# Performance work log

Hardware: AMD Instinct MI355X
Metric: run time of the kernel (lower is better)

Reference implementation:

```python
import jax, jax.numpy as jnp
from jax import lax
import numpy as np

T_STEPS, C_IN, H_IN, W_IN = 15, 6, 256, 256
C_OUT, KSIZE = 64, 5
THRESH = 15.0   # conv_t[0]
KWTA = 5        # ks[0]
INH_R = 3       # inh_radiuses[0]


def setup_inputs() -> dict:
    key = jax.random.key(0)
    k1, k2 = jax.random.split(key)
    # cumulative binary spike-wave: once a unit spikes it stays on (SpykeTorch convention)
    bern = jax.random.uniform(k1, (T_STEPS, C_IN, H_IN, W_IN)) < 0.05
    spikes = (jnp.cumsum(bern.astype(jnp.int32), axis=0) > 0).astype(jnp.float32)
    # SpykeTorch Convolution init: N(0.8, 0.05)
    w1 = 0.8 + 0.05 * jax.random.normal(k2, (C_OUT, C_IN, KSIZE, KSIZE), dtype=jnp.float32)
    return {"input": spikes, "w1": w1, "current_layer_id": 1}


def pointwise_inhibition(thr_pot):
    # thr_pot: (T, C, H, W). Keep, at each spatial position, only the feature
    # with the earliest spike (ties broken by max potential); zero the rest.
    T = thr_pot.shape[0]
    C = thr_pot.shape[1]
    max_vals = jnp.max(thr_pot, axis=1, keepdims=True)            # (T,1,H,W)
    max_idx = jnp.argmax(thr_pot, axis=1, keepdims=True)          # (T,1,H,W)
    clamp_pot = jnp.sign(max_vals)                                # (T,1,H,W) in {0,1}
    earliest = jnp.clip((T - clamp_pot.sum(axis=0, keepdims=True)).astype(jnp.int32), 0, T - 1)  # (1,1,H,W)
    winners = jnp.take_along_axis(max_idx, earliest, axis=0)      # (1,1,H,W)
    onehot = (jnp.arange(C)[None, :, None, None] == winners[:, 0])  # (1,C,H,W)
    coef = onehot.astype(thr_pot.dtype) * clamp_pot[-1:]          # zero where no spike at last step
    return thr_pot * coef


def get_k_winners(pot, spk, kwta, inh_radius):
    # pot, spk: (T, C, H, W). Returns (kwta, 3) int winners (c, h, w); -1 rows = no winner.
    T, C, H, W = pot.shape
    earliest = jnp.clip((T - spk.sum(axis=0, keepdims=True)).astype(jnp.int32), 0, T - 1)
    values = jnp.take_along_axis(pot, earliest, axis=0)           # (1,C,H,W)
    trunc = spk * values
    v = trunc.max() * T
    trunc = trunc + spk * v
    total = trunc.sum(axis=0)                                     # (C,H,W)
    rows = jnp.arange(H)
    cols = jnp.arange(W)

    def step(total, _):
        idx = jnp.argmax(total)
        val = total.reshape(-1)[idx]
        c = idx // (H * W)
        rem = idx % (H * W)
        h = rem // W
        w = rem % W
        winner = jnp.where(val != 0,
                           jnp.stack([c, h, w]),
                           jnp.full((3,), -1, dtype=idx.dtype))
        total = total.at[c].set(0.0)
        box = (((rows >= h - inh_radius) & (rows <= h + inh_radius))[:, None]
               & ((cols >= w - inh_radius) & (cols <= w + inh_radius))[None, :])
        total = jnp.where(box[None, :, :], 0.0, total)            # columnar spatial inhibition
        return total, winner

    _, winners = lax.scan(step, total, None, length=kwta)
    return winners


def reference(input, w1, current_layer_id):
    # training path, current_layer_id == 1
    x = jnp.pad(input.astype(jnp.float32), ((0, 0), (0, 0), (2, 2), (2, 2)))  # sf.pad (2,2,2,2)
    pot = lax.conv_general_dilated(x, w1, (1, 1), 'VALID',
                                   dimension_numbers=('NCHW', 'OIHW', 'NCHW'))  # (T,64,256,256)
    pot = jnp.where(pot < THRESH, 0.0, pot)   # sf.fire -> thresholded potentials
    pot = pointwise_inhibition(pot)
    spk = jnp.sign(pot)
    winners = get_k_winners(pot, spk, KWTA, INH_R)
    return spk, pot, winners
```

## Files before the change

### kernel.cpp

```cpp
#include <hip/hip_runtime.h>
#include <stdint.h>

static constexpr int T_STEPS = 15;
static constexpr int C_IN = 6;
static constexpr int C_OUT = 64;
static constexpr int H = 256;
static constexpr int W = 256;
static constexpr int NPOS = H * W;
static constexpr int NTAP = 150;
#define DTHRESH 15.0

typedef float vfloat4 __attribute__((ext_vector_type(4)));

static constexpr size_t WS_FT     = 0;
static constexpr size_t WS_SERIES = 393216;
static constexpr size_t WS_WINC   = WS_SERIES + (size_t)NPOS*16*4;
static constexpr size_t WS_NMAP   = WS_WINC + (size_t)NPOS;
static constexpr size_t WS_VAL    = WS_NMAP + (size_t)NPOS;
static constexpr size_t WS_NEED   = WS_VAL + (size_t)NPOS*8;

__global__ __launch_bounds__(256) void ft_kernel(const float* __restrict__ x,
                                                 uint8_t* __restrict__ ft) {
    int i = blockIdx.x * 256 + threadIdx.x;
    if (i >= C_IN * NPOS) return;
    int f = 15;
    #pragma unroll
    for (int t = T_STEPS - 1; t >= 0; --t) {
        if (x[(size_t)t * (C_IN * NPOS) + i] > 0.0f) f = t;
    }
    ft[i] = (uint8_t)f;
}

__global__ __launch_bounds__(256, 4) void conv_kernel(
        const float* __restrict__ w1, const uint8_t* __restrict__ ftg,
        float* __restrict__ series_ws, int8_t* __restrict__ winc_ws,
        uint8_t* __restrict__ nmap_ws, double* __restrict__ val_ws)
{
    __shared__ float w_lds[NTAP * 64];
    __shared__ uint8_t ft_lds[6 * 5 * 20];
    __shared__ alignas(16) unsigned cnt_lds[4][16];
    __shared__ alignas(16) unsigned short sorted_lds[4][200];

    int tid = threadIdx.x;
    int bid = blockIdx.x;
    int h  = bid >> 4;
    int w0 = (bid & 15) << 4;

    for (int i = tid; i < C_OUT * NTAP; i += 256) {
        int o = i / NTAP;
        int tap = i - o * NTAP;
        w_lds[tap * 64 + o] = w1[i];
    }
    for (int i = tid; i < 600; i += 256) {
        int c = i / 100;
        int r = i - c * 100;
        int kh = r / 20;
        int j  = r - kh * 20;
        int gh = h - 2 + kh;
        int gw = w0 - 2 + j;
        uint8_t v = 15;
        if (gh >= 0 && gh < H && gw >= 0 && gw < W) v = ftg[c * NPOS + gh * W + gw];
        ft_lds[(c * 5 + kh) * 20 + j] = v;
    }
    __syncthreads();

    int lane = tid & 63;
    int wvi  = tid >> 6;
    unsigned* cnt = cnt_lds[wvi];
    unsigned short* srt = sorted_lds[wvi];

    for (int iter = 0; iter < 4; ++iter) {
        int xl = iter * 4 + wvi;
        int p  = h * W + w0 + xl;

        if (lane < 16) cnt[lane] = 0;

        int tap0 = lane, tap1 = lane + 64, tap2 = lane + 128;
        auto ftv = [&](int tap) -> unsigned {
            int c = tap / 25;
            int r = tap - c * 25;
            int kh = r / 5;
            int kw = r - kh * 5;
            return ft_lds[(c * 5 + kh) * 20 + xl + kw];
        };
        unsigned f0 = ftv(tap0);
        unsigned f1 = ftv(tap1);
        unsigned f2 = (tap2 < NTAP) ? ftv(tap2) : 15u;
        unsigned r0 = 0, r1 = 0, r2 = 0;
        if (f0 < 15u) r0 = atomicAdd(&cnt[f0], 1u);
        if (f1 < 15u) r1 = atomicAdd(&cnt[f1], 1u);
        if (f2 < 15u) r2 = atomicAdd(&cnt[f2], 1u);

        uint4 c4[4];
        #pragma unroll
        for (int i = 0; i < 4; ++i) c4[i] = ((const uint4*)cnt)[i];
        unsigned cv_t[16];
        #pragma unroll
        for (int i = 0; i < 4; ++i) {
            cv_t[4*i+0] = c4[i].x; cv_t[4*i+1] = c4[i].y;
            cv_t[4*i+2] = c4[i].z; cv_t[4*i+3] = c4[i].w;
        }
        int kt[15];
        #pragma unroll
        for (int t = 0; t < 15; ++t) kt[t] = (int)__builtin_amdgcn_readfirstlane(cv_t[t]);

        unsigned st0 = 0, st1 = 0, st2 = 0;
        #pragma unroll
        for (int t = 0; t < 15; ++t) {
            unsigned a = (cv_t[t] + 3u) & ~3u;
            if ((unsigned)t < f0) st0 += a;
            if ((unsigned)t < f1) st1 += a;
            if ((unsigned)t < f2) st2 += a;
        }
        if (f0 < 15u) srt[st0 + r0] = (unsigned short)(tap0 << 6);
        if (f1 < 15u) srt[st1 + r1] = (unsigned short)(tap1 << 6);
        if (f2 < 15u) srt[st2 + r2] = (unsigned short)(tap2 << 6);

        double run = 0.0, cvv = 0.0;
        int tc = 127;
        float ser[15];
        int A = 0;
        #pragma unroll
        for (int t = 0; t < 15; ++t) {
            int k = kt[t];
            for (int q = 0; q < k; q += 4) {
                uint2 pr = *(const uint2*)(srt + A + q);
                unsigned e0 = pr.x & 0xFFFFu, e1 = pr.x >> 16;
                unsigned e2 = pr.y & 0xFFFFu, e3 = pr.y >> 16;
                e0 = min(e0, 9536u); e1 = min(e1, 9536u);
                e2 = min(e2, 9536u); e3 = min(e3, 9536u);
                float wa = w_lds[e0 + lane];
                float wb = w_lds[e1 + lane];
                float wcf = w_lds[e2 + lane];
                float wd = w_lds[e3 + lane];
                double p0 = (double)wa;
                double p1 = (q + 1 < k) ? (double)wb : 0.0;
                double p2 = (q + 2 < k) ? (double)wcf : 0.0;
                double p3 = (q + 3 < k) ? (double)wd : 0.0;
                run += ((p0 + p1) + (p2 + p3));
            }
            A += (k + 3) & ~3;
            ser[t] = (float)run;
            bool cross_now = (tc == 127) && (run >= DTHRESH);
            if (cross_now) { tc = t; cvv = run; }
        }

        int e = tc;
        #pragma unroll
        for (int off = 32; off >= 1; off >>= 1) e = min(e, __shfl_xor(e, off));
        int wc = -1;
        double val = 0.0;
        if (e < 15) {
            double vl = (tc == e) ? cvv : 0.0;
            double m = vl;
            #pragma unroll
            for (int off = 32; off >= 1; off >>= 1) m = fmax(m, __shfl_xor(m, off));
            unsigned long long mk = __ballot(vl == m);
            wc = __ffsll(mk) - 1;
            val = m;

            float ov = 0.0f;
            #pragma unroll
            for (int t = 0; t < 15; ++t) {
                float sv = __shfl(ser[t], wc);
                if (lane == t) ov = sv;
            }
            if (lane < e) ov = 0.0f;
            if (lane < 15) series_ws[p * 16 + lane] = ov;
        }
        if (lane == 0) {
            winc_ws[p] = (int8_t)wc;
            nmap_ws[p] = (uint8_t)(wc >= 0 ? (15 - e) : 0);
            if (wc >= 0) val_ws[p] = val;
        }
    }
}

__global__ __launch_bounds__(1024) void kwin_kernel(
        const int8_t* __restrict__ winc, const uint8_t* __restrict__ nmap,
        const double* __restrict__ val, float* __restrict__ outw)
{
    __shared__ int8_t  winc_l[NPOS];
    __shared__ uint8_t nmap_l[NPOS];
    __shared__ double rv_lds[16];
    __shared__ unsigned ri_lds[16];
    __shared__ double v_lds;
    __shared__ int win_c[5], win_h[5], win_w[5];
    int tid = threadIdx.x, lane = tid & 63, wvi = tid >> 6;

    {
        const int4* ws4 = (const int4*)winc;
        int4* wd4 = (int4*)winc_l;
        const int4* ns4 = (const int4*)nmap;
        int4* nd4 = (int4*)nmap_l;
        #pragma unroll
        for (int i = 0; i < NPOS / 16 / 1024; ++i) {
            wd4[tid + (i << 10)] = ws4[tid + (i << 10)];
            nd4[tid + (i << 10)] = ns4[tid + (i << 10)];
        }
    }
    __syncthreads();

    double mv = 0.0;
    for (int k = 0; k < 64; ++k) {
        int p = (k << 10) + tid;
        if (winc_l[p] >= 0) mv = fmax(mv, val[p]);
    }
    #pragma unroll
    for (int off = 32; off >= 1; off >>= 1) mv = fmax(mv, __shfl_xor(mv, off));
    if (lane == 0) rv_lds[wvi] = mv;
    __syncthreads();
    if (tid == 0) {
        double m = rv_lds[0];
        for (int i = 1; i < 16; ++i) m = fmax(m, rv_lds[i]);
        v_lds = 15.0 * m;
    }
    __syncthreads();
    double v = v_lds;

    for (int r = 0; r < 5; ++r) {
        int pc[5], ph[5], pw[5];
        #pragma unroll
        for (int j = 0; j < 5; ++j) { pc[j] = (j < r) ? win_c[j] : -99;
                                      ph[j] = (j < r) ? win_h[j] : -99;
                                      pw[j] = (j < r) ? win_w[j] : -99; }
        double bv = -1.0;
        unsigned bi = 0xFFFFFFFFu;
        for (int k = 0; k < 64; ++k) {
            int p = (k << 10) + tid;
            int c = winc_l[p];
            bool alive = (c >= 0);
            int hh = p >> 8, ww = p & 255;
            #pragma unroll
            for (int j = 0; j < 5; ++j) {
                bool kill = (c == pc[j]) ||
                            (hh >= ph[j] - 3 && hh <= ph[j] + 3 &&
                             ww >= pw[j] - 3 && ww <= pw[j] + 3);
                alive = alive && !kill;
            }
            if (alive) {
                double tot = (double)nmap_l[p] * (val[p] + v);
                unsigned fi = ((unsigned)c << 16) | (unsigned)p;
                if (tot > bv || (tot == bv && fi < bi)) { bv = tot; bi = fi; }
            }
        }
        #pragma unroll
        for (int off = 32; off >= 1; off >>= 1) {
            double ov = __shfl_xor(bv, off);
            unsigned oi = __shfl_xor(bi, off);
            if (ov > bv || (ov == bv && oi < bi)) { bv = ov; bi = oi; }
        }
        if (lane == 0) { rv_lds[wvi] = bv; ri_lds[wvi] = bi; }
        __syncthreads();
        if (tid == 0) {
            double bbv = rv_lds[0]; unsigned bbi = ri_lds[0];
            for (int i = 1; i < 16; ++i) {
                double ov = rv_lds[i]; unsigned oi = ri_lds[i];
                if (ov > bbv || (ov == bbv && oi < bbi)) { bbv = ov; bbi = oi; }
            }
            bool valid = (bbv > 0.0);
            int c = (int)(bbi >> 16), pp = (int)(bbi & 0xFFFFu);
            int hh = pp >> 8, ww = pp & 255;
            outw[r * 3 + 0] = valid ? (float)c  : -1.0f;
            outw[r * 3 + 1] = valid ? (float)hh : -1.0f;
            outw[r * 3 + 2] = valid ? (float)ww : -1.0f;
            win_c[r] = c; win_h[r] = hh; win_w[r] = ww;
        }
        __syncthreads();
    }
}

__global__ __launch_bounds__(256) void expand_kernel(
        const int8_t* __restrict__ winc, const float* __restrict__ series,
        float* __restrict__ spk, float* __restrict__ pot)
{
    int idx4 = blockIdx.x * 256 + threadIdx.x;
    int w4 = idx4 & 63;
    int h  = (idx4 >> 6) & 255;
    int c  = (idx4 >> 14) & 63;
    int t  = idx4 >> 20;
    int pbase = h * W + (w4 << 2);
    uint32_t wcs = *reinterpret_cast<const uint32_t*>(winc + pbase);
    vfloat4 pv = (vfloat4)(0.0f);
    vfloat4 sv = (vfloat4)(0.0f);
    #pragma unroll
    for (int e2 = 0; e2 < 4; ++e2) {
        int8_t wcb = (int8_t)((wcs >> (8 * e2)) & 0xFFu);
        if ((int)wcb == c) {
            float xv = series[(size_t)(pbase + e2) * 16 + t];
            pv[e2] = xv;
            sv[e2] = (xv > 0.f) ? 1.0f : 0.0f;
        }
    }
    reinterpret_cast<vfloat4*>(spk)[idx4] = sv;
    reinterpret_cast<vfloat4*>(pot)[idx4] = pv;
}

extern "C" void kernel_launch(void* const* d_in, const int* in_sizes, int n_in,
                              void* d_out, int out_size, void* d_ws, size_t ws_size,
                              hipStream_t stream)
{
    if (ws_size < WS_NEED) return;

    const float* x  = (const float*)d_in[0];
    const float* w1 = (const float*)d_in[1];
    uint8_t* ws = (uint8_t*)d_ws;
    uint8_t* ftg    = ws + WS_FT;
    float*   series = (float*)(ws + WS_SERIES);
    int8_t*  winc   = (int8_t*)(ws + WS_WINC);
    uint8_t* nmap   = (uint8_t*)(ws + WS_NMAP);
    double*  val    = (double*)(ws + WS_VAL);

    float* spk  = (float*)d_out;
    float* pot  = spk + (size_t)T_STEPS * C_OUT * NPOS;
    float* outw = pot + (size_t)T_STEPS * C_OUT * NPOS;

    hipLaunchKernelGGL(ft_kernel,     dim3(1536),  dim3(256),  0, stream, x, ftg);
    hipLaunchKernelGGL(conv_kernel,   dim3(4096),  dim3(256),  0, stream, w1, ftg, series, winc, nmap, val);
    hipLaunchKernelGGL(kwin_kernel,   dim3(1),     dim3(1024), 0, stream, winc, nmap, val, outw);
    hipLaunchKernelGGL(expand_kernel, dim3(61440), dim3(256),  0, stream, winc, series, spk, pot);
}
```

Before: 868.9 us.

## Merge k-winner selection into expand kernel so both run concurrently

```diff
diff --git a/kernel.cpp b/kernel.cpp
--- a/kernel.cpp
+++ b/kernel.cpp
@@ -176,35 +176,46 @@
     }
 }
 
-__global__ __launch_bounds__(1024) void kwin_kernel(
+__global__ __launch_bounds__(1024) void kwin_expand_kernel(
         const int8_t* __restrict__ winc, const uint8_t* __restrict__ nmap,
-        const double* __restrict__ val, float* __restrict__ outw)
+        const double* __restrict__ val, const float* __restrict__ series,
+        float* __restrict__ spk, float* __restrict__ pot, float* __restrict__ outw)
 {
-    __shared__ int8_t  winc_l[NPOS];
-    __shared__ uint8_t nmap_l[NPOS];
+    int tid = threadIdx.x;
+    if (blockIdx.x != 0) {
+        int idx4 = (blockIdx.x - 1) * 1024 + tid;
+        int w4 = idx4 & 63;
+        int h  = (idx4 >> 6) & 255;
+        int c  = (idx4 >> 14) & 63;
+        int t  = idx4 >> 20;
+        int pbase = h * W + (w4 << 2);
+        uint32_t wcs = *reinterpret_cast<const uint32_t*>(winc + pbase);
+        vfloat4 pv = (vfloat4)(0.0f);
+        vfloat4 sv = (vfloat4)(0.0f);
+        #pragma unroll
+        for (int e2 = 0; e2 < 4; ++e2) {
+            int8_t wcb = (int8_t)((wcs >> (8 * e2)) & 0xFFu);
+            if ((int)wcb == c) {
+                float xv = series[(size_t)(pbase + e2) * 16 + t];
+                pv[e2] = xv;
+                sv[e2] = (xv > 0.f) ? 1.0f : 0.0f;
+            }
+        }
+        reinterpret_cast<vfloat4*>(spk)[idx4] = sv;
+        reinterpret_cast<vfloat4*>(pot)[idx4] = pv;
+        return;
+    }
+
     __shared__ double rv_lds[16];
     __shared__ unsigned ri_lds[16];
     __shared__ double v_lds;
     __shared__ int win_c[5], win_h[5], win_w[5];
-    int tid = threadIdx.x, lane = tid & 63, wvi = tid >> 6;
-
-    {
-        const int4* ws4 = (const int4*)winc;
-        int4* wd4 = (int4*)winc_l;
-        const int4* ns4 = (const int4*)nmap;
-        int4* nd4 = (int4*)nmap_l;
-        #pragma unroll
-        for (int i = 0; i < NPOS / 16 / 1024; ++i) {
-            wd4[tid + (i << 10)] = ws4[tid + (i << 10)];
-            nd4[tid + (i << 10)] = ns4[tid + (i << 10)];
-        }
-    }
-    __syncthreads();
+    int lane = tid & 63, wvi = tid >> 6;
 
     double mv = 0.0;
     for (int k = 0; k < 64; ++k) {
         int p = (k << 10) + tid;
-        if (winc_l[p] >= 0) mv = fmax(mv, val[p]);
+        if (winc[p] >= 0) mv = fmax(mv, val[p]);
     }
     #pragma unroll
     for (int off = 32; off >= 1; off >>= 1) mv = fmax(mv, __shfl_xor(mv, off));
@@ -228,7 +239,7 @@
         unsigned bi = 0xFFFFFFFFu;
         for (int k = 0; k < 64; ++k) {
             int p = (k << 10) + tid;
-            int c = winc_l[p];
+            int c = winc[p];
             bool alive = (c >= 0);
             int hh = p >> 8, ww = p & 255;
             #pragma unroll
@@ -239,7 +250,7 @@
                 alive = alive && !kill;
             }
             if (alive) {
-                double tot = (double)nmap_l[p] * (val[p] + v);
+                double tot = (double)nmap[p] * (val[p] + v);
                 unsigned fi = ((unsigned)c << 16) | (unsigned)p;
                 if (tot > bv || (tot == bv && fi < bi)) { bv = tot; bi = fi; }
             }
@@ -268,32 +279,6 @@
         }
         __syncthreads();
     }
-}
-
-__global__ __launch_bounds__(256) void expand_kernel(
-        const int8_t* __restrict__ winc, const float* __restrict__ series,
-        float* __restrict__ spk, float* __restrict__ pot)
-{
-    int idx4 = blockIdx.x * 256 + threadIdx.x;
-    int w4 = idx4 & 63;
-    int h  = (idx4 >> 6) & 255;
-    int c  = (idx4 >> 14) & 63;
-    int t  = idx4 >> 20;
-    int pbase = h * W + (w4 << 2);
-    uint32_t wcs = *reinterpret_cast<const uint32_t*>(winc + pbase);
-    vfloat4 pv = (vfloat4)(0.0f);
-    vfloat4 sv = (vfloat4)(0.0f);
-    #pragma unroll
-    for (int e2 = 0; e2 < 4; ++e2) {
-        int8_t wcb = (int8_t)((wcs >> (8 * e2)) & 0xFFu);
-        if ((int)wcb == c) {
-            float xv = series[(size_t)(pbase + e2) * 16 + t];
-            pv[e2] = xv;
-            sv[e2] = (xv > 0.f) ? 1.0f : 0.0f;
-        }
-    }
-    reinterpret_cast<vfloat4*>(spk)[idx4] = sv;
-    reinterpret_cast<vfloat4*>(pot)[idx4] = pv;
 }
 
 extern "C" void kernel_launch(void* const* d_in, const int* in_sizes, int n_in,
@@ -315,8 +300,8 @@
     float* pot  = spk + (size_t)T_STEPS * C_OUT * NPOS;
     float* outw = pot + (size_t)T_STEPS * C_OUT * NPOS;
 
-    hipLaunchKernelGGL(ft_kernel,     dim3(1536),  dim3(256),  0, stream, x, ftg);
-    hipLaunchKernelGGL(conv_kernel,   dim3(4096),  dim3(256),  0, stream, w1, ftg, series, winc, nmap, val);
-    hipLaunchKernelGGL(kwin_kernel,   dim3(1),     dim3(1024), 0, stream, winc, nmap, val, outw);
-    hipLaunchKernelGGL(expand_kernel, dim3(61440), dim3(256),  0, stream, winc, series, spk, pot);
+    hipLaunchKernelGGL(ft_kernel,   dim3(1536), dim3(256),  0, stream, x, ftg);
+    hipLaunchKernelGGL(conv_kernel, dim3(4096), dim3(256),  0, stream, w1, ftg, series, winc, nmap, val);
+    hipLaunchKernelGGL(kwin_expand_kernel, dim3(15361), dim3(1024), 0, stream,
+                       winc, nmap, val, series, spk, pot, outw);
 }
```

New measurement: 904.1 us. +4.1%, slower.
